# Kernel optimization log

Measured on AMD Instinct MI355X. Metric: run time of the kernel, lower is better.

The kernel has to match this reference:

```python
import jax, jax.numpy as jnp
import numpy as np

INPUT_SIZE = 8
WINDOW = 128
HIDDEN = 256
B, T = 1024, 256

def _cell(W_ih, W_hh, b_ih, b_hh, h, c, x):
    # PyTorch LSTM gate order: i, f, g, o
    gates = x @ W_ih.T + h @ W_hh.T + b_ih + b_hh  # [B, 4H]
    i, f, g, o = jnp.split(gates, 4, axis=-1)
    c = jax.nn.sigmoid(f) * c + jax.nn.sigmoid(i) * jnp.tanh(g)
    h = jax.nn.sigmoid(o) * jnp.tanh(c)
    return h, c

def setup_inputs() -> dict:
    key = jax.random.key(0)
    ks = jax.random.split(key, 12)
    s = 1.0 / np.sqrt(HIDDEN)
    u = lambda k, shape: jax.random.uniform(k, shape, jnp.float32, -s, s)
    return {
        'x': jax.random.normal(ks[0], (B, T, INPUT_SIZE), jnp.float32),
        'W_ih0': u(ks[1], (4 * HIDDEN, INPUT_SIZE)),
        'W_hh0': u(ks[2], (4 * HIDDEN, HIDDEN)),
        'b_ih0': u(ks[3], (4 * HIDDEN,)),
        'b_hh0': u(ks[4], (4 * HIDDEN,)),
        'W_ih1': u(ks[5], (4 * HIDDEN, HIDDEN)),
        'W_hh1': u(ks[6], (4 * HIDDEN, HIDDEN)),
        'b_ih1': u(ks[7], (4 * HIDDEN,)),
        'b_hh1': u(ks[8], (4 * HIDDEN,)),
        'W_lin': u(ks[9], (1, HIDDEN)),
        'b_lin': u(ks[10], (1,)),
    }

def reference(x, W_ih0, W_hh0, b_ih0, b_hh0, W_ih1, W_hh1, b_ih1, b_hh1, W_lin, b_lin):
    Bx = x.shape[0]
    h0 = jnp.zeros((Bx, HIDDEN), x.dtype)
    params = [(W_ih0, W_hh0, b_ih0, b_hh0), (W_ih1, W_hh1, b_ih1, b_hh1)]

    # ---- warmup: multi-layer LSTM over first WINDOW steps ----
    x_pre = jnp.swapaxes(x[:, :WINDOW], 0, 1)   # [W, B, in]
    x_post = jnp.swapaxes(x[:, WINDOW:, 1:], 0, 1)  # [T-W, B, in-1]

    hs, cs = [], []
    seq = x_pre
    for (Wi, Wh, bi, bh) in params:
        def step(carry, xt, Wi=Wi, Wh=Wh, bi=bi, bh=bh):
            h, c = carry
            h, c = _cell(Wi, Wh, bi, bh, h, c, xt)
            return (h, c), h
        (hT, cT), seq = jax.lax.scan(step, (h0, h0), seq)
        hs.append(hT); cs.append(cT)

    pred0 = hs[-1] @ W_lin.T + b_lin  # [B, 1]

    def ar_step(carry, xt_rest):
        h0_, c0_, h1_, c1_, pred = carry
        xin = jnp.concatenate([pred, xt_rest], axis=1)  # [B, in]
        h0_, c0_ = _cell(W_ih0, W_hh0, b_ih0, b_hh0, h0_, c0_, xin)
        h1_, c1_ = _cell(W_ih1, W_hh1, b_ih1, b_hh1, h1_, c1_, h0_)
        pred = h1_ @ W_lin.T + b_lin
        return (h0_, c0_, h1_, c1_, pred), pred

    carry0 = (hs[0], cs[0], hs[1], cs[1], pred0)
    _, preds = jax.lax.scan(ar_step, carry0, x_post)  # [T-W, B, 1]

    out = jnp.concatenate([pred0[None], preds], axis=0)  # [T-W+1, B, 1]
    return jnp.swapaxes(out, 0, 1)  # [B, T-W+1, 1]
```

## Files before the change

kernel.cpp:

```cpp
#include <hip/hip_runtime.h>
#include <cstdint>

#define HID  256
#define NG   1024
#define TT   256
#define WIN  128
#define K0   264
#define K1   512
#define OUTW 129

__device__ __forceinline__ float sigm(float z)  { return 1.0f / (1.0f + __expf(-z)); }
__device__ __forceinline__ float tanhx(float z) { float e = __expf(2.0f * z); return 1.0f - 2.0f / (e + 1.0f); }

__global__ void prep_kernel(const float* __restrict__ Wih0, const float* __restrict__ Whh0,
                            const float* __restrict__ bih0, const float* __restrict__ bhh0,
                            const float* __restrict__ Wih1, const float* __restrict__ Whh1,
                            const float* __restrict__ bih1, const float* __restrict__ bhh1,
                            float* __restrict__ ws) {
  const int n0 = K0 * NG, n1 = K1 * NG;
  const int total = n0 + n1 + 2 * NG;
  for (int i = blockIdx.x * blockDim.x + threadIdx.x; i < total; i += gridDim.x * blockDim.x) {
    float v;
    if (i < n0) {
      int k = i >> 10, g = i & (NG - 1);
      v = (k < 8) ? Wih0[g * 8 + k] : Whh0[g * HID + (k - 8)];
    } else if (i < n0 + n1) {
      int j = i - n0;
      int k = j >> 10, g = j & (NG - 1);
      v = (k < HID) ? Wih1[g * HID + k] : Whh1[g * HID + (k - HID)];
    } else if (i < n0 + n1 + NG) {
      int g = i - n0 - n1;
      v = bih0[g] + bhh0[g];
    } else {
      int g = i - n0 - n1 - NG;
      v = bih1[g] + bhh1[g];
    }
    ws[i] = v;
  }
}

__global__ __launch_bounds__(256) void lstm_ar_kernel(
    const float* __restrict__ x, const float* __restrict__ Wlin,
    const float* __restrict__ blin, const float* __restrict__ ws,
    float* __restrict__ out)
{
  const float* __restrict__ WT0 = ws;
  const float* __restrict__ WT1 = ws + K0 * NG;
  const float* __restrict__ bs0 = ws + (K0 + K1) * NG;
  const float* __restrict__ bs1 = bs0 + NG;

  __shared__ float in0[K0][4];
  __shared__ float in1[K1][4];
  __shared__ float c0s[HID][4];
  __shared__ float c1s[HID][4];
  __shared__ float gl[4][NG];
  __shared__ float predl[4];

  const int tid = threadIdx.x;
  const int r0  = blockIdx.x << 2;

  {
    float4 z = make_float4(0.f, 0.f, 0.f, 0.f);
    *(float4*)&c0s[tid][0]       = z;
    *(float4*)&c1s[tid][0]       = z;
    *(float4*)&in0[8 + tid][0]   = z;
    *(float4*)&in1[tid][0]       = z;
    *(float4*)&in1[HID + tid][0] = z;
  }
  __syncthreads();

  for (int t = 0; t < TT; ++t) {
    if (tid < 32) {
      int r = tid >> 3, k = tid & 7;
      float v;
      if (t >= WIN && k == 0) v = predl[r];
      else v = x[((size_t)(r0 + r) * TT + t) * 8 + k];
      in0[k][r] = v;
    }
    __syncthreads();

    {
      const int g4 = tid << 2;
      float4 b = *(const float4*)&bs0[g4];
      float4 a0 = b, a1 = b, a2 = b, a3 = b;
      #pragma unroll 4
      for (int k = 0; k < K0; ++k) {
        const float4 w = *(const float4*)&WT0[(k << 10) + g4];
        const float4 h = *(const float4*)&in0[k][0];
        a0.x += w.x * h.x; a0.y += w.y * h.x; a0.z += w.z * h.x; a0.w += w.w * h.x;
        a1.x += w.x * h.y; a1.y += w.y * h.y; a1.z += w.z * h.y; a1.w += w.w * h.y;
        a2.x += w.x * h.z; a2.y += w.y * h.z; a2.z += w.z * h.z; a2.w += w.w * h.z;
        a3.x += w.x * h.w; a3.y += w.y * h.w; a3.z += w.z * h.w; a3.w += w.w * h.w;
      }
      *(float4*)&gl[0][g4] = a0;
      *(float4*)&gl[1][g4] = a1;
      *(float4*)&gl[2][g4] = a2;
      *(float4*)&gl[3][g4] = a3;
    }
    __syncthreads();

    {
      const int j = tid;
      float4 c = *(const float4*)&c0s[j][0];
      float cc[4] = {c.x, c.y, c.z, c.w};
      float hh[4];
      #pragma unroll
      for (int r = 0; r < 4; ++r) {
        float ig = sigm(gl[r][j]);
        float fg = sigm(gl[r][HID + j]);
        float gg = tanhx(gl[r][2 * HID + j]);
        float og = sigm(gl[r][3 * HID + j]);
        float cn = fg * cc[r] + ig * gg;
        cc[r] = cn;
        hh[r] = og * tanhx(cn);
      }
      *(float4*)&c0s[j][0] = make_float4(cc[0], cc[1], cc[2], cc[3]);
      float4 hv = make_float4(hh[0], hh[1], hh[2], hh[3]);
      *(float4*)&in0[8 + j][0] = hv;
      *(float4*)&in1[j][0]     = hv;
    }
    __syncthreads();

    {
      const int g4 = tid << 2;
      float4 b = *(const float4*)&bs1[g4];
      float4 a0 = b, a1 = b, a2 = b, a3 = b;
      #pragma unroll 4
      for (int k = 0; k < K1; ++k) {
        const float4 w = *(const float4*)&WT1[(k << 10) + g4];
        const float4 h = *(const float4*)&in1[k][0];
        a0.x += w.x * h.x; a0.y += w.y * h.x; a0.z += w.z * h.x; a0.w += w.w * h.x;
        a1.x += w.x * h.y; a1.y += w.y * h.y; a1.z += w.z * h.y; a1.w += w.w * h.y;
        a2.x += w.x * h.z; a2.y += w.y * h.z; a2.z += w.z * h.z; a2.w += w.w * h.z;
        a3.x += w.x * h.w; a3.y += w.y * h.w; a3.z += w.z * h.w; a3.w += w.w * h.w;
      }
      *(float4*)&gl[0][g4] = a0;
      *(float4*)&gl[1][g4] = a1;
      *(float4*)&gl[2][g4] = a2;
      *(float4*)&gl[3][g4] = a3;
    }
    __syncthreads();

    {
      const int j = tid;
      float4 c = *(const float4*)&c1s[j][0];
      float cc[4] = {c.x, c.y, c.z, c.w};
      float hh[4];
      #pragma unroll
      for (int r = 0; r < 4; ++r) {
        float ig = sigm(gl[r][j]);
        float fg = sigm(gl[r][HID + j]);
        float gg = tanhx(gl[r][2 * HID + j]);
        float og = sigm(gl[r][3 * HID + j]);
        float cn = fg * cc[r] + ig * gg;
        cc[r] = cn;
        hh[r] = og * tanhx(cn);
      }
      *(float4*)&c1s[j][0] = make_float4(cc[0], cc[1], cc[2], cc[3]);
      *(float4*)&in1[HID + j][0] = make_float4(hh[0], hh[1], hh[2], hh[3]);
    }
    __syncthreads();

    if (t >= WIN - 1) {
      const int w = tid >> 6, l = tid & 63;
      float s = 0.f;
      #pragma unroll
      for (int q = 0; q < 4; ++q) {
        int j = l + (q << 6);
        s += Wlin[j] * in1[HID + j][w];
      }
      #pragma unroll
      for (int off = 32; off; off >>= 1) s += __shfl_down(s, off);
      if (l == 0) {
        float p = s + blin[0];
        predl[w] = p;
        out[(size_t)(r0 + w) * OUTW + (t - (WIN - 1))] = p;
      }
    }
    __syncthreads();
  }
}

extern "C" void kernel_launch(void* const* d_in, const int* in_sizes, int n_in,
                              void* d_out, int out_size, void* d_ws, size_t ws_size,
                              hipStream_t stream) {
  (void)in_sizes; (void)n_in; (void)out_size; (void)ws_size;
  const float* x    = (const float*)d_in[0];
  const float* Wih0 = (const float*)d_in[1];
  const float* Whh0 = (const float*)d_in[2];
  const float* bih0 = (const float*)d_in[3];
  const float* bhh0 = (const float*)d_in[4];
  const float* Wih1 = (const float*)d_in[5];
  const float* Whh1 = (const float*)d_in[6];
  const float* bih1 = (const float*)d_in[7];
  const float* bhh1 = (const float*)d_in[8];
  const float* Wlin = (const float*)d_in[9];
  const float* blin = (const float*)d_in[10];
  float* ws  = (float*)d_ws;
  float* out = (float*)d_out;

  prep_kernel<<<256, 256, 0, stream>>>(Wih0, Whh0, bih0, bhh0,
                                       Wih1, Whh1, bih1, bhh1, ws);
  lstm_ar_kernel<<<256, 256, 0, stream>>>(x, Wlin, blin, ws, out);
}
```

Baseline: 10.38 ms.

## Rewrite LSTM recurrence on MFMA with split-fp16 weights and 16 rows per block

```diff
diff --git a/kernel.cpp b/kernel.cpp
--- a/kernel.cpp
+++ b/kernel.cpp
@@ -1,185 +1,215 @@
 #include <hip/hip_runtime.h>
 #include <cstdint>
 
-#define HID  256
-#define NG   1024
-#define TT   256
-#define WIN  128
-#define K0   264
-#define K1   512
+#define HID 256
+#define NG 1024
+#define TT 256
+#define WIN 128
 #define OUTW 129
+#define NBLK 64
+#define ROWS 16
+#define NTHR 1024
+#define KK0 9
+#define KK1 16
+#define GLP 1044
+
+typedef _Float16 half8 __attribute__((ext_vector_type(8)));
+typedef float f32x4 __attribute__((ext_vector_type(4)));
+
+#define W0H (KK0 * 65536)
+#define W1H (KK1 * 65536)
 
 __device__ __forceinline__ float sigm(float z)  { return 1.0f / (1.0f + __expf(-z)); }
 __device__ __forceinline__ float tanhx(float z) { float e = __expf(2.0f * z); return 1.0f - 2.0f / (e + 1.0f); }
 
-__global__ void prep_kernel(const float* __restrict__ Wih0, const float* __restrict__ Whh0,
-                            const float* __restrict__ bih0, const float* __restrict__ bhh0,
-                            const float* __restrict__ Wih1, const float* __restrict__ Whh1,
-                            const float* __restrict__ bih1, const float* __restrict__ bhh1,
-                            float* __restrict__ ws) {
-  const int n0 = K0 * NG, n1 = K1 * NG;
-  const int total = n0 + n1 + 2 * NG;
+__device__ __forceinline__ void split_f(float v, _Float16& hi, _Float16& lo) {
+  float h = (fabsf(v) < 0.0009765625f) ? 0.0f : (float)(_Float16)v;
+  hi = (_Float16)h;
+  lo = (_Float16)((v - h) * 2048.0f);
+}
+
+__device__ __forceinline__ int aidx(int k, int r) {
+  return ((k >> 5) * 64 + ((k >> 3) & 3) * 16 + r) * 8 + (k & 7);
+}
+
+__global__ void prep_pack(const float* __restrict__ Wih0, const float* __restrict__ Whh0,
+                          const float* __restrict__ Wih1, const float* __restrict__ Whh1,
+                          _Float16* __restrict__ wp) {
+  const int total = W0H + W1H;
   for (int i = blockIdx.x * blockDim.x + threadIdx.x; i < total; i += gridDim.x * blockDim.x) {
-    float v;
-    if (i < n0) {
-      int k = i >> 10, g = i & (NG - 1);
-      v = (k < 8) ? Wih0[g * 8 + k] : Whh0[g * HID + (k - 8)];
-    } else if (i < n0 + n1) {
-      int j = i - n0;
-      int k = j >> 10, g = j & (NG - 1);
-      v = (k < HID) ? Wih1[g * HID + k] : Whh1[g * HID + (k - HID)];
-    } else if (i < n0 + n1 + NG) {
-      int g = i - n0 - n1;
-      v = bih0[g] + bhh0[g];
+    int layer, kk, rem;
+    if (i < W0H) { layer = 0; kk = i >> 16; rem = i & 65535; }
+    else { int j = i - W0H; layer = 1; kk = j >> 16; rem = j & 65535; }
+    const int nt    = rem >> 10;
+    const int plane = (rem >> 9) & 1;
+    const int lane  = (rem >> 3) & 63;
+    const int j8    = rem & 7;
+    const int k = kk * 32 + ((lane >> 4) << 3) + j8;
+    const int n = nt * 16 + (lane & 15);
+    float w;
+    if (layer == 0) {
+      if (k < 8)        w = Wih0[n * 8 + k];
+      else if (k < 264) w = Whh0[n * 256 + (k - 8)];
+      else              w = 0.0f;
     } else {
-      int g = i - n0 - n1 - NG;
-      v = bih1[g] + bhh1[g];
-    }
-    ws[i] = v;
-  }
-}
-
-__global__ __launch_bounds__(256) void lstm_ar_kernel(
-    const float* __restrict__ x, const float* __restrict__ Wlin,
-    const float* __restrict__ blin, const float* __restrict__ ws,
-    float* __restrict__ out)
+      if (k < 256)      w = Wih1[n * 256 + k];
+      else              w = Whh1[n * 256 + (k - 256)];
+    }
+    _Float16 hi, lo; split_f(w, hi, lo);
+    wp[i] = plane ? lo : hi;
+  }
+}
+
+template<int KK>
+__device__ __forceinline__ void gate_phase(const _Float16* __restrict__ wB,
+                                           const _Float16* __restrict__ sAh,
+                                           const _Float16* __restrict__ sAl,
+                                           float* __restrict__ sGl,
+                                           int wv, int lane) {
+  f32x4 zz = {0.f, 0.f, 0.f, 0.f};
+  f32x4 a0[4], a1[4], a2[4];
+  #pragma unroll
+  for (int i = 0; i < 4; ++i) { a0[i] = zz; a1[i] = zz; a2[i] = zz; }
+  for (int kk = 0; kk < KK; ++kk) {
+    const half8 ah = *(const half8*)(sAh + kk * 512 + lane * 8);
+    const half8 al = *(const half8*)(sAl + kk * 512 + lane * 8);
+    const _Float16* bp = wB + (size_t)kk * 65536 + (size_t)(wv * 4) * 1024 + lane * 8;
+    #pragma unroll
+    for (int i = 0; i < 4; ++i) {
+      const half8 bh = *(const half8*)(bp + i * 1024);
+      const half8 bl = *(const half8*)(bp + i * 1024 + 512);
+      a0[i] = __builtin_amdgcn_mfma_f32_16x16x32_f16(ah, bh, a0[i], 0, 0, 0);
+      a1[i] = __builtin_amdgcn_mfma_f32_16x16x32_f16(ah, bl, a1[i], 0, 0, 0);
+      a2[i] = __builtin_amdgcn_mfma_f32_16x16x32_f16(al, bh, a2[i], 0, 0, 0);
+    }
+  }
+  const int dr0 = (lane >> 4) << 2;
+  const int dc  = lane & 15;
+  #pragma unroll
+  for (int i = 0; i < 4; ++i) {
+    const int col = (wv * 4 + i) * 16 + dc;
+    #pragma unroll
+    for (int r = 0; r < 4; ++r)
+      sGl[(dr0 + r) * GLP + col] = a0[i][r] + 4.8828125e-4f * (a1[i][r] + a2[i][r]);
+  }
+}
+
+__global__ __launch_bounds__(NTHR, 4) void lstm_mfma(
+    const float* __restrict__ x,
+    const float* __restrict__ bih0, const float* __restrict__ bhh0,
+    const float* __restrict__ bih1, const float* __restrict__ bhh1,
+    const float* __restrict__ Wlin, const float* __restrict__ blin,
+    const _Float16* __restrict__ wp, float* __restrict__ out)
 {
-  const float* __restrict__ WT0 = ws;
-  const float* __restrict__ WT1 = ws + K0 * NG;
-  const float* __restrict__ bs0 = ws + (K0 + K1) * NG;
-  const float* __restrict__ bs1 = bs0 + NG;
-
-  __shared__ float in0[K0][4];
-  __shared__ float in1[K1][4];
-  __shared__ float c0s[HID][4];
-  __shared__ float c1s[HID][4];
-  __shared__ float gl[4][NG];
-  __shared__ float predl[4];
-
-  const int tid = threadIdx.x;
-  const int r0  = blockIdx.x << 2;
+  extern __shared__ char smraw[];
+  _Float16* sA0h = (_Float16*)smraw;
+  _Float16* sA0l = sA0h + 4608;
+  _Float16* sA1h = sA0l + 4608;
+  _Float16* sA1l = sA1h + 8192;
+  float* sGl  = (float*)(smraw + 51200);
+  float* sH1  = sGl + 16 * GLP;
+  float* sWlin = sH1 + ROWS * HID;
+
+  const int tid  = threadIdx.x;
+  const int lane = tid & 63;
+  const int wv   = tid >> 6;
+  const int r0   = blockIdx.x * ROWS;
+
+  const int eu = (tid >> 2) & 255;
+  const int ef = tid & 3;
+
+  for (int i = tid; i < 3200; i += NTHR) ((int4*)smraw)[i] = make_int4(0, 0, 0, 0);
+  if (tid < HID) sWlin[tid] = Wlin[tid];
+
+  const float b0i = bih0[eu]       + bhh0[eu];
+  const float b0f = bih0[eu + 256] + bhh0[eu + 256];
+  const float b0g = bih0[eu + 512] + bhh0[eu + 512];
+  const float b0o = bih0[eu + 768] + bhh0[eu + 768];
+  const float b1i = bih1[eu]       + bhh1[eu];
+  const float b1f = bih1[eu + 256] + bhh1[eu + 256];
+  const float b1g = bih1[eu + 512] + bhh1[eu + 512];
+  const float b1o = bih1[eu + 768] + bhh1[eu + 768];
+  const float blv = blin[0];
+  float c0s[4] = {0.f, 0.f, 0.f, 0.f}, c1s[4] = {0.f, 0.f, 0.f, 0.f};
+  __syncthreads();
+
+  for (int t = 0; t < TT; ++t) {
+    if (t >= WIN) {
+      const float4 wl4 = *(const float4*)&sWlin[lane << 2];
+      const float4 h4  = *(const float4*)&sH1[(wv << 8) + (lane << 2)];
+      float s = wl4.x * h4.x + wl4.y * h4.y + wl4.z * h4.z + wl4.w * h4.w;
+      #pragma unroll
+      for (int m = 1; m < 64; m <<= 1) s += __shfl_xor(s, m);
+      if (lane == 0) {
+        const float pv = s + blv;
+        out[(size_t)(r0 + wv) * OUTW + (t - WIN)] = pv;
+        _Float16 hh, hl; split_f(pv, hh, hl);
+        sA0h[wv << 3] = hh; sA0l[wv << 3] = hl;
+      }
+    }
+    if (tid < 128) {
+      const int r = tid >> 3, f = tid & 7;
+      if (f > 0 || t < WIN) {
+        const float v = x[((size_t)(r0 + r) * TT + t) * 8 + f];
+        _Float16 hh, hl; split_f(v, hh, hl);
+        const int ai = r * 8 + f;
+        sA0h[ai] = hh; sA0l[ai] = hl;
+      }
+    }
+    __syncthreads();
+
+    gate_phase<KK0>(wp, sA0h, sA0l, sGl, wv, lane);
+    __syncthreads();
+
+    #pragma unroll
+    for (int q = 0; q < 4; ++q) {
+      const int r = ef + (q << 2);
+      const float gi = sGl[r * GLP + eu]       + b0i;
+      const float gf = sGl[r * GLP + eu + 256] + b0f;
+      const float gg = sGl[r * GLP + eu + 512] + b0g;
+      const float go = sGl[r * GLP + eu + 768] + b0o;
+      const float c  = sigm(gf) * c0s[q] + sigm(gi) * tanhx(gg);
+      c0s[q] = c;
+      const float h = sigm(go) * tanhx(c);
+      _Float16 hh, hl; split_f(h, hh, hl);
+      const int i1 = aidx(eu, r), i0 = aidx(eu + 8, r);
+      sA1h[i1] = hh; sA1l[i1] = hl;
+      sA0h[i0] = hh; sA0l[i0] = hl;
+    }
+    __syncthreads();
+
+    gate_phase<KK1>(wp + W0H, sA1h, sA1l, sGl, wv, lane);
+    __syncthreads();
+
+    #pragma unroll
+    for (int q = 0; q < 4; ++q) {
+      const int r = ef + (q << 2);
+      const float gi = sGl[r * GLP + eu]       + b1i;
+      const float gf = sGl[r * GLP + eu + 256] + b1f;
+      const float gg = sGl[r * GLP + eu + 512] + b1g;
+      const float go = sGl[r * GLP + eu + 768] + b1o;
+      const float c  = sigm(gf) * c1s[q] + sigm(gi) * tanhx(gg);
+      c1s[q] = c;
+      const float h = sigm(go) * tanhx(c);
+      _Float16 hh, hl; split_f(h, hh, hl);
+      const int i1 = aidx(HID + eu, r);
+      sA1h[i1] = hh; sA1l[i1] = hl;
+      sH1[r * HID + eu] = h;
+    }
+    __syncthreads();
+  }
 
   {
-    float4 z = make_float4(0.f, 0.f, 0.f, 0.f);
-    *(float4*)&c0s[tid][0]       = z;
-    *(float4*)&c1s[tid][0]       = z;
-    *(float4*)&in0[8 + tid][0]   = z;
-    *(float4*)&in1[tid][0]       = z;
-    *(float4*)&in1[HID + tid][0] = z;
-  }
-  __syncthreads();
-
-  for (int t = 0; t < TT; ++t) {
-    if (tid < 32) {
-      int r = tid >> 3, k = tid & 7;
-      float v;
-      if (t >= WIN && k == 0) v = predl[r];
-      else v = x[((size_t)(r0 + r) * TT + t) * 8 + k];
-      in0[k][r] = v;
-    }
-    __syncthreads();
-
-    {
-      const int g4 = tid << 2;
-      float4 b = *(const float4*)&bs0[g4];
-      float4 a0 = b, a1 = b, a2 = b, a3 = b;
-      #pragma unroll 4
-      for (int k = 0; k < K0; ++k) {
-        const float4 w = *(const float4*)&WT0[(k << 10) + g4];
-        const float4 h = *(const float4*)&in0[k][0];
-        a0.x += w.x * h.x; a0.y += w.y * h.x; a0.z += w.z * h.x; a0.w += w.w * h.x;
-        a1.x += w.x * h.y; a1.y += w.y * h.y; a1.z += w.z * h.y; a1.w += w.w * h.y;
-        a2.x += w.x * h.z; a2.y += w.y * h.z; a2.z += w.z * h.z; a2.w += w.w * h.z;
-        a3.x += w.x * h.w; a3.y += w.y * h.w; a3.z += w.z * h.w; a3.w += w.w * h.w;
-      }
-      *(float4*)&gl[0][g4] = a0;
-      *(float4*)&gl[1][g4] = a1;
-      *(float4*)&gl[2][g4] = a2;
-      *(float4*)&gl[3][g4] = a3;
-    }
-    __syncthreads();
-
-    {
-      const int j = tid;
-      float4 c = *(const float4*)&c0s[j][0];
-      float cc[4] = {c.x, c.y, c.z, c.w};
-      float hh[4];
-      #pragma unroll
-      for (int r = 0; r < 4; ++r) {
-        float ig = sigm(gl[r][j]);
-        float fg = sigm(gl[r][HID + j]);
-        float gg = tanhx(gl[r][2 * HID + j]);
-        float og = sigm(gl[r][3 * HID + j]);
-        float cn = fg * cc[r] + ig * gg;
-        cc[r] = cn;
-        hh[r] = og * tanhx(cn);
-      }
-      *(float4*)&c0s[j][0] = make_float4(cc[0], cc[1], cc[2], cc[3]);
-      float4 hv = make_float4(hh[0], hh[1], hh[2], hh[3]);
-      *(float4*)&in0[8 + j][0] = hv;
-      *(float4*)&in1[j][0]     = hv;
-    }
-    __syncthreads();
-
-    {
-      const int g4 = tid << 2;
-      float4 b = *(const float4*)&bs1[g4];
-      float4 a0 = b, a1 = b, a2 = b, a3 = b;
-      #pragma unroll 4
-      for (int k = 0; k < K1; ++k) {
-        const float4 w = *(const float4*)&WT1[(k << 10) + g4];
-        const float4 h = *(const float4*)&in1[k][0];
-        a0.x += w.x * h.x; a0.y += w.y * h.x; a0.z += w.z * h.x; a0.w += w.w * h.x;
-        a1.x += w.x * h.y; a1.y += w.y * h.y; a1.z += w.z * h.y; a1.w += w.w * h.y;
-        a2.x += w.x * h.z; a2.y += w.y * h.z; a2.z += w.z * h.z; a2.w += w.w * h.z;
-        a3.x += w.x * h.w; a3.y += w.y * h.w; a3.z += w.z * h.w; a3.w += w.w * h.w;
-      }
-      *(float4*)&gl[0][g4] = a0;
-      *(float4*)&gl[1][g4] = a1;
-      *(float4*)&gl[2][g4] = a2;
-      *(float4*)&gl[3][g4] = a3;
-    }
-    __syncthreads();
-
-    {
-      const int j = tid;
-      float4 c = *(const float4*)&c1s[j][0];
-      float cc[4] = {c.x, c.y, c.z, c.w};
-      float hh[4];
-      #pragma unroll
-      for (int r = 0; r < 4; ++r) {
-        float ig = sigm(gl[r][j]);
-        float fg = sigm(gl[r][HID + j]);
-        float gg = tanhx(gl[r][2 * HID + j]);
-        float og = sigm(gl[r][3 * HID + j]);
-        float cn = fg * cc[r] + ig * gg;
-        cc[r] = cn;
-        hh[r] = og * tanhx(cn);
-      }
-      *(float4*)&c1s[j][0] = make_float4(cc[0], cc[1], cc[2], cc[3]);
-      *(float4*)&in1[HID + j][0] = make_float4(hh[0], hh[1], hh[2], hh[3]);
-    }
-    __syncthreads();
-
-    if (t >= WIN - 1) {
-      const int w = tid >> 6, l = tid & 63;
-      float s = 0.f;
-      #pragma unroll
-      for (int q = 0; q < 4; ++q) {
-        int j = l + (q << 6);
-        s += Wlin[j] * in1[HID + j][w];
-      }
-      #pragma unroll
-      for (int off = 32; off; off >>= 1) s += __shfl_down(s, off);
-      if (l == 0) {
-        float p = s + blin[0];
-        predl[w] = p;
-        out[(size_t)(r0 + w) * OUTW + (t - (WIN - 1))] = p;
-      }
-    }
-    __syncthreads();
-  }
-}
+    const float4 wl4 = *(const float4*)&sWlin[lane << 2];
+    const float4 h4  = *(const float4*)&sH1[(wv << 8) + (lane << 2)];
+    float s = wl4.x * h4.x + wl4.y * h4.y + wl4.z * h4.z + wl4.w * h4.w;
+    #pragma unroll
+    for (int m = 1; m < 64; m <<= 1) s += __shfl_xor(s, m);
+    if (lane == 0) out[(size_t)(r0 + wv) * OUTW + 128] = s + blv;
+  }
+}
+
+#define SMEM_BYTES 135424
 
 extern "C" void kernel_launch(void* const* d_in, const int* in_sizes, int n_in,
                               void* d_out, int out_size, void* d_ws, size_t ws_size,
@@ -196,10 +226,13 @@
   const float* bhh1 = (const float*)d_in[8];
   const float* Wlin = (const float*)d_in[9];
   const float* blin = (const float*)d_in[10];
-  float* ws  = (float*)d_ws;
+  _Float16* wp = (_Float16*)d_ws;
   float* out = (float*)d_out;
 
-  prep_kernel<<<256, 256, 0, stream>>>(Wih0, Whh0, bih0, bhh0,
-                                       Wih1, Whh1, bih1, bhh1, ws);
-  lstm_ar_kernel<<<256, 256, 0, stream>>>(x, Wlin, blin, ws, out);
-}
+  prep_pack<<<2048, 256, 0, stream>>>(Wih0, Whh0, Wih1, Whh1, wp);
+
+  (void)hipFuncSetAttribute(reinterpret_cast<const void*>(lstm_mfma),
+                            hipFuncAttributeMaxDynamicSharedMemorySize, SMEM_BYTES);
+  lstm_mfma<<<NBLK, NTHR, SMEM_BYTES, stream>>>(x, bih0, bhh0, bih1, bhh1,
+                                                Wlin, blin, wp, out);
+}
```

New measurement: 30.60 ms. 195% more time.
